# Kernel tuning notes

Measured on AMD Instinct MI355X. Metric: run time of the kernel, lower is better.

## Reference

```python
import jax, jax.numpy as jnp
import numpy as np

B, T, H, NH = 2, 2048, 1024, 16
HD = H // NH


def setup_inputs() -> dict:
    key = jax.random.key(0)
    ks = jax.random.split(key, 12)
    s = 1.0 / np.sqrt(H)
    inp = {
        "q": jax.random.normal(ks[0], (B, T, H), jnp.float32),
        "k": jax.random.normal(ks[1], (B, T, H), jnp.float32),
        "v": jax.random.normal(ks[2], (B, T, H), jnp.float32),
        "mask": jnp.tril(jnp.ones((T, T), jnp.int32))[None, None],  # causal [1,1,T,T]
        "w_q": jax.random.normal(ks[3], (H, H), jnp.float32) * s,
        "b_q": jax.random.normal(ks[4], (H,), jnp.float32) * 0.01,
        "w_k": jax.random.normal(ks[5], (H, H), jnp.float32) * s,
        "b_k": jax.random.normal(ks[6], (H,), jnp.float32) * 0.01,
        "w_v": jax.random.normal(ks[7], (H, H), jnp.float32) * s,
        "b_v": jax.random.normal(ks[8], (H,), jnp.float32) * 0.01,
        "w_o": jax.random.normal(ks[9], (H, H), jnp.float32) * s,
        "b_o": jax.random.normal(ks[10], (H,), jnp.float32) * 0.01,
    }
    return inp


def reference(q, k, v, mask, w_q, b_q, w_k, b_k, w_v, b_v, w_o, b_o):
    def split_heads(x):
        Bx, Tx, _ = x.shape
        return x.reshape(Bx, Tx, NH, HD).transpose(0, 2, 1, 3)  # [B,NH,T,HD]

    Q = split_heads(q @ w_q.T + b_q)
    K = split_heads(k @ w_k.T + b_k)
    V = split_heads(v @ w_v.T + b_v)

    scores = jnp.einsum("bhqd,bhkd->bhqk", Q, K) / np.sqrt(HD).astype(np.float32)
    scores = jnp.where(mask == 0, jnp.float32(-1e9), scores)
    weights = jax.nn.softmax(scores, axis=-1)  # dropout prob = 0.0
    out = jnp.einsum("bhqk,bhkd->bhqd", weights, V)
    out = out.transpose(0, 2, 1, 3).reshape(q.shape[0], q.shape[1], H)
    return out @ w_o.T + b_o
```

## Files before the change

### kernel.cpp

```cpp
#include <hip/hip_runtime.h>
#include <hip/hip_bf16.h>

#define Bb 2
#define Tt 2048
#define Hh 1024
#define NHh 16

typedef short bf16x8 __attribute__((ext_vector_type(8)));
typedef float f32x4 __attribute__((ext_vector_type(4)));
typedef unsigned short u16;
typedef unsigned int u32;
typedef u16 u16x4v __attribute__((ext_vector_type(4)));
typedef u32 u32x2v __attribute__((ext_vector_type(2)));

#define QK_SCALE 0.180336880f

#if __has_builtin(__builtin_amdgcn_exp2f)
__device__ __forceinline__ float exp2_fast(float x) { return __builtin_amdgcn_exp2f(x); }
#else
__device__ __forceinline__ float exp2_fast(float x) { return __expf(x * 0.69314718f); }
#endif

__device__ __forceinline__ u16 f2b(float x) {
  unsigned u = __builtin_bit_cast(unsigned, x);
  u += 0x7FFFu + ((u >> 16) & 1u);
  return (u16)(u >> 16);
}

__device__ __forceinline__ u32 cvt_pk(float lo, float hi) {
  u32 r;
  asm("v_cvt_pk_bf16_f32 %0, %1, %2" : "=v"(r) : "v"(lo), "v"(hi));
  return r;
}

__global__ __launch_bounds__(256) void cvt_all_kernel(
    const float* __restrict__ q, const float* __restrict__ k, const float* __restrict__ v,
    const float* __restrict__ wq, const float* __restrict__ wk,
    const float* __restrict__ wv, const float* __restrict__ wo,
    u16* __restrict__ qb, u16* __restrict__ kb, u16* __restrict__ vb,
    u16* __restrict__ wqb, u16* __restrict__ wkb, u16* __restrict__ wvb,
    u16* __restrict__ wob, int n4_in, int n4_w) {
  const int which = blockIdx.y;
  const float* src;
  u16* dst;
  int n4;
  float sc = 1.0f;
  switch (which) {
    case 0: src = q;  dst = qb;  n4 = n4_in; break;
    case 1: src = k;  dst = kb;  n4 = n4_in; break;
    case 2: src = v;  dst = vb;  n4 = n4_in; break;
    case 3: src = wq; dst = wqb; n4 = n4_w; sc = QK_SCALE; break;
    case 4: src = wk; dst = wkb; n4 = n4_w; break;
    case 5: src = wv; dst = wvb; n4 = n4_w; break;
    default: src = wo; dst = wob; n4 = n4_w; break;
  }
  int i = blockIdx.x * blockDim.x + threadIdx.x;
  int stride = gridDim.x * blockDim.x;
  for (; i < n4; i += stride) {
    float4 vv = ((const float4*)src)[i];
    u16x4v o;
    o.x = f2b(vv.x * sc); o.y = f2b(vv.y * sc); o.z = f2b(vv.z * sc); o.w = f2b(vv.w * sc);
    ((u16x4v*)dst)[i] = o;
  }
}

template<int NF, int MODE>
__device__ __forceinline__ void gemm_body(const u16* __restrict__ A,
                                          const u16* __restrict__ W,
                                          const float* __restrict__ bias, float bscale,
                                          void* __restrict__ Cout,
                                          u16* lA, u16* lB, int mt, int nt) {
  const int tid = threadIdx.x;
  const int lane = tid & 63;
  const int wid = tid >> 6;
  const int wr = wid >> 1, wc = wid & 1;
  const int g = lane >> 4, fr = lane & 15;
  constexpr int NT = NF * 32;

  f32x4 acc[4][NF];
#pragma unroll
  for (int m = 0; m < 4; ++m)
#pragma unroll
    for (int n = 0; n < NF; ++n) acc[m][n] = (f32x4){0.f, 0.f, 0.f, 0.f};

  const int srow = tid >> 3;
  const int scol = (tid & 7) * 8;

  bf16x8 ra[4], rb[NF];
#pragma unroll
  for (int ps = 0; ps < 4; ++ps)
    ra[ps] = *(const bf16x8*)(A + (size_t)(mt * 128 + ps * 32 + srow) * Hh + scol);
#pragma unroll
  for (int ps = 0; ps < NF; ++ps)
    rb[ps] = *(const bf16x8*)(W + (size_t)(nt * NT + ps * 32 + srow) * Hh + scol);
#pragma unroll
  for (int ps = 0; ps < 4; ++ps) {
    int r = ps * 32 + srow;
    *(bf16x8*)((char*)lA + r * 128 + ((scol * 2) ^ ((r & 7) << 4))) = ra[ps];
  }
#pragma unroll
  for (int ps = 0; ps < NF; ++ps) {
    int r = ps * 32 + srow;
    *(bf16x8*)((char*)lB + r * 128 + ((scol * 2) ^ ((r & 7) << 4))) = rb[ps];
  }
  __syncthreads();

  for (int kt = 0; kt < Hh; kt += 64) {
    if (kt + 64 < Hh) {
#pragma unroll
      for (int ps = 0; ps < 4; ++ps)
        ra[ps] = *(const bf16x8*)(A + (size_t)(mt * 128 + ps * 32 + srow) * Hh + kt + 64 + scol);
#pragma unroll
      for (int ps = 0; ps < NF; ++ps)
        rb[ps] = *(const bf16x8*)(W + (size_t)(nt * NT + ps * 32 + srow) * Hh + kt + 64 + scol);
    }
    bf16x8 af[4][2], bfv[NF][2];
#pragma unroll
    for (int m = 0; m < 4; ++m)
#pragma unroll
      for (int ks = 0; ks < 2; ++ks) {
        int r = wr * 64 + m * 16 + fr;
        af[m][ks] = *(const bf16x8*)((const char*)lA + r * 128 + ((ks * 64 + g * 16) ^ ((r & 7) << 4)));
      }
#pragma unroll
    for (int n = 0; n < NF; ++n)
#pragma unroll
      for (int ks = 0; ks < 2; ++ks) {
        int r = wc * (NT / 2) + n * 16 + fr;
        bfv[n][ks] = *(const bf16x8*)((const char*)lB + r * 128 + ((ks * 64 + g * 16) ^ ((r & 7) << 4)));
      }
#pragma unroll
    for (int m = 0; m < 4; ++m)
#pragma unroll
      for (int n = 0; n < NF; ++n)
#pragma unroll
        for (int ks = 0; ks < 2; ++ks)
          acc[m][n] = __builtin_amdgcn_mfma_f32_16x16x32_bf16(af[m][ks], bfv[n][ks],
                                                              acc[m][n], 0, 0, 0);
    if (kt + 64 < Hh) {
      __syncthreads();
#pragma unroll
      for (int ps = 0; ps < 4; ++ps) {
        int r = ps * 32 + srow;
        *(bf16x8*)((char*)lA + r * 128 + ((scol * 2) ^ ((r & 7) << 4))) = ra[ps];
      }
#pragma unroll
      for (int ps = 0; ps < NF; ++ps) {
        int r = ps * 32 + srow;
        *(bf16x8*)((char*)lB + r * 128 + ((scol * 2) ^ ((r & 7) << 4))) = rb[ps];
      }
      __syncthreads();
    }
  }

#pragma unroll
  for (int n = 0; n < NF; ++n) {
    int Cc = nt * NT + wc * (NT / 2) + n * 16 + fr;
    float bv = bias[Cc] * bscale;
#pragma unroll
    for (int m = 0; m < 4; ++m) {
#pragma unroll
      for (int j = 0; j < 4; ++j) {
        int R = mt * 128 + wr * 64 + m * 16 + g * 4 + j;
        float val = acc[m][n][j] + bv;
        if constexpr (MODE == 0) {
          int bb = R >> 11, t = R & (Tt - 1);
          int h = Cc >> 6, d = Cc & 63;
          ((u16*)Cout)[(((size_t)(bb * NHh + h) * Tt + t) << 6) + d] = f2b(val);
        } else if constexpr (MODE == 2) {
          int bb = R >> 11, t = R & (Tt - 1);
          int h = Cc >> 6, d = Cc & 63;
          ((u16*)Cout)[(((size_t)(bb * NHh + h) * 64 + d) << 11) + t] = f2b(val);
        } else {
          ((float*)Cout)[(size_t)R * Hh + Cc] = val;
        }
      }
    }
  }
}

__global__ __launch_bounds__(256, 4) void proj_qkv_kernel(
    const u16* __restrict__ qb, const u16* __restrict__ kb, const u16* __restrict__ vb,
    const u16* __restrict__ wqb, const u16* __restrict__ wkb, const u16* __restrict__ wvb,
    const float* __restrict__ biq, const float* __restrict__ bik, const float* __restrict__ biv,
    u16* __restrict__ Qp, u16* __restrict__ Kp, u16* __restrict__ Vt) {
  __shared__ u16 lA[128 * 64];
  __shared__ u16 lB[64 * 64];
  const int id = blockIdx.x;
  const int j = id >> 3;
  const int slot = (id & 7) + 8 * (j >> 4);
  const int nt = j & 15;
  const int z = slot >> 5, mt = slot & 31;
  if (z == 0)      gemm_body<2, 0>(qb, wqb, biq, QK_SCALE, Qp, lA, lB, mt, nt);
  else if (z == 1) gemm_body<2, 0>(kb, wkb, bik, 1.0f, Kp, lA, lB, mt, nt);
  else             gemm_body<2, 2>(vb, wvb, biv, 1.0f, Vt, lA, lB, mt, nt);
}

__global__ __launch_bounds__(256, 2) void gemm_out_kernel(
    const u16* __restrict__ A, const u16* __restrict__ W,
    const float* __restrict__ bias, float* __restrict__ Cout) {
  __shared__ u16 lA[128 * 64];
  __shared__ u16 lB[64 * 64];
  const int id = blockIdx.x;
  const int j = id >> 3;
  const int mt = (id & 7) + 8 * (j >> 4);
  const int nt = j & 15;
  gemm_body<2, 1>(A, W, bias, 1.0f, Cout, lA, lB, mt, nt);
}

__global__ __launch_bounds__(256, 6) void attn_kernel(const u16* __restrict__ Qp,
                                                      const u16* __restrict__ Kp,
                                                      const u16* __restrict__ Vt,
                                                      u16* __restrict__ AO) {
  __shared__ u16 lK[64 * 64];
  __shared__ u16 lV[64 * 64];
  __shared__ u16 lP[64 * 64];
  const int tid = threadIdx.x;
  const int lane = tid & 63;
  const int w = tid >> 6;
  const int g = lane >> 4, fr = lane & 15;
  const int L = blockIdx.x;
  const int i = L & 255, k4 = L >> 8;
  const int bh = i & 31, s8 = i >> 5;
  const int t2 = s8 * 2 + (k4 >> 1);
  const int qt = (k4 & 1) ? (31 - t2) : t2;
  const int q0 = qt * 64;

  bf16x8 qf[2];
  {
    const u16* qrow = Qp + (((size_t)bh * Tt + q0 + w * 16 + fr) << 6) + g * 8;
    qf[0] = *(const bf16x8*)(qrow);
    qf[1] = *(const bf16x8*)(qrow + 32);
  }

  const int srow = tid >> 3;
  const int scol = (tid & 7) * 8;
  const int sswz = (scol * 2) ^ ((srow & 7) << 4);

  bf16x8 rk[2], rv[2];
#pragma unroll
  for (int ps = 0; ps < 2; ++ps) {
    rk[ps] = *(const bf16x8*)(Kp + (((size_t)bh * Tt + ps * 32 + srow) << 6) + scol);
    rv[ps] = *(const bf16x8*)(Vt + (((size_t)bh * 64 + ps * 32 + srow) << 11) + scol);
  }
#pragma unroll
  for (int ps = 0; ps < 2; ++ps) {
    *(bf16x8*)((char*)lK + (ps * 32 + srow) * 128 + sswz) = rk[ps];
    *(bf16x8*)((char*)lV + (ps * 32 + srow) * 128 + sswz) = rv[ps];
  }
  __syncthreads();

  float m_r = -1e30f, l_r = 0.f;
  f32x4 acc[4];
#pragma unroll
  for (int nd = 0; nd < 4; ++nd) acc[nd] = (f32x4){0.f, 0.f, 0.f, 0.f};

  const int prow = w * 16 + fr;
  const int psw = (prow & 7) << 4;
  const int qoff = w * 16 + fr;

  for (int jt = 0; jt <= qt; ++jt) {
    if (jt < qt) {
#pragma unroll
      for (int ps = 0; ps < 2; ++ps) {
        rk[ps] = *(const bf16x8*)(Kp + (((size_t)bh * Tt + (jt + 1) * 64 + ps * 32 + srow) << 6) + scol);
        rv[ps] = *(const bf16x8*)(Vt + (((size_t)bh * 64 + ps * 32 + srow) << 11) + (jt + 1) * 64 + scol);
      }
    }
    f32x4 s[4];
    __builtin_amdgcn_s_setprio(1);
#pragma unroll
    for (int n = 0; n < 4; ++n) {
      s[n] = (f32x4){0.f, 0.f, 0.f, 0.f};
      int rbase = (n * 16 + fr) * 128;
      int rsw = (fr & 7) << 4;
#pragma unroll
      for (int ks = 0; ks < 2; ++ks) {
        bf16x8 ak = *(const bf16x8*)((const char*)lK + rbase + ((ks * 64 + g * 16) ^ rsw));
        s[n] = __builtin_amdgcn_mfma_f32_16x16x32_bf16(ak, qf[ks], s[n], 0, 0, 0);
      }
    }
    __builtin_amdgcn_s_setprio(0);

    float tm = -1e30f;
    if (jt == qt) {
#pragma unroll
      for (int n = 0; n < 4; ++n)
#pragma unroll
        for (int r = 0; r < 4; ++r) {
          if (n * 16 + g * 4 + r > qoff) s[n][r] = -1e30f;
          tm = fmaxf(tm, s[n][r]);
        }
    } else {
#pragma unroll
      for (int n = 0; n < 4; ++n)
#pragma unroll
        for (int r = 0; r < 4; ++r) tm = fmaxf(tm, s[n][r]);
    }
    tm = fmaxf(tm, __shfl_xor(tm, 16));
    tm = fmaxf(tm, __shfl_xor(tm, 32));
    if (!__all(tm <= m_r + 8.0f)) {
      float mn = fmaxf(m_r, tm);
      float sc = exp2_fast(m_r - mn);
      m_r = mn;
      l_r *= sc;
      float scj[4];
#pragma unroll
      for (int j = 0; j < 4; ++j) scj[j] = __shfl(sc, g * 4 + j);
#pragma unroll
      for (int nd = 0; nd < 4; ++nd)
#pragma unroll
        for (int j = 0; j < 4; ++j) acc[nd][j] *= scj[j];
    }
    float rs = 0.f;
    u32 pw[4][2];
#pragma unroll
    for (int n = 0; n < 4; ++n) {
      float p0 = exp2_fast(s[n][0] - m_r);
      float p1 = exp2_fast(s[n][1] - m_r);
      float p2 = exp2_fast(s[n][2] - m_r);
      float p3 = exp2_fast(s[n][3] - m_r);
      rs += (p0 + p1) + (p2 + p3);
      pw[n][0] = cvt_pk(p0, p1);
      pw[n][1] = cvt_pk(p2, p3);
    }
    rs += __shfl_xor(rs, 16);
    rs += __shfl_xor(rs, 32);
    l_r += rs;
    bf16x8 pa[2];
    {
      char* base = (char*)lP + prow * 128;
#pragma unroll
      for (int n = 0; n < 4; ++n)
        *(u32x2v*)(base + ((32 * n + 8 * g) ^ psw)) = (u32x2v){pw[n][0], pw[n][1]};
#pragma unroll
      for (int ks = 0; ks < 2; ++ks)
        pa[ks] = *(const bf16x8*)(base + ((ks * 64 + g * 16) ^ psw));
    }
    __builtin_amdgcn_s_setprio(1);
#pragma unroll
    for (int nd = 0; nd < 4; ++nd) {
      int rbase = (nd * 16 + fr) * 128;
      int rsw = (fr & 7) << 4;
#pragma unroll
      for (int ks = 0; ks < 2; ++ks) {
        bf16x8 bv = *(const bf16x8*)((const char*)lV + rbase + ((ks * 64 + g * 16) ^ rsw));
        acc[nd] = __builtin_amdgcn_mfma_f32_16x16x32_bf16(pa[ks], bv, acc[nd], 0, 0, 0);
      }
    }
    __builtin_amdgcn_s_setprio(0);
    if (jt < qt) {
      __syncthreads();
#pragma unroll
      for (int ps = 0; ps < 2; ++ps) {
        *(bf16x8*)((char*)lK + (ps * 32 + srow) * 128 + sswz) = rk[ps];
        *(bf16x8*)((char*)lV + (ps * 32 + srow) * 128 + sswz) = rv[ps];
      }
      __syncthreads();
    }
  }

  const int b = bh >> 4, hh = bh & 15;
  float lj[4];
#pragma unroll
  for (int j = 0; j < 4; ++j) lj[j] = __shfl(l_r, g * 4 + j);
#pragma unroll
  for (int j = 0; j < 4; ++j) {
    float inv = 1.0f / lj[j];
    int qq = q0 + w * 16 + g * 4 + j;
    size_t base = (((size_t)b * Tt + qq) << 10) + hh * 64;
#pragma unroll
    for (int nd = 0; nd < 4; ++nd)
      AO[base + nd * 16 + fr] = f2b(acc[nd][j] * inv);
  }
}

extern "C" void kernel_launch(void* const* d_in, const int* in_sizes, int n_in,
                              void* d_out, int out_size, void* d_ws, size_t ws_size,
                              hipStream_t stream) {
  const float* q   = (const float*)d_in[0];
  const float* k   = (const float*)d_in[1];
  const float* v   = (const float*)d_in[2];
  const float* wq  = (const float*)d_in[4];
  const float* bq  = (const float*)d_in[5];
  const float* wk  = (const float*)d_in[6];
  const float* bk  = (const float*)d_in[7];
  const float* wv  = (const float*)d_in[8];
  const float* bv  = (const float*)d_in[9];
  const float* wo  = (const float*)d_in[10];
  const float* bo  = (const float*)d_in[11];

  char* ws = (char*)d_ws;
  const size_t SZB = (size_t)Bb * Tt * Hh * 2;
  const size_t WB  = (size_t)Hh * Hh * 2;
  u16* qb  = (u16*)(ws);
  u16* kb  = (u16*)(ws + SZB);
  u16* vb  = (u16*)(ws + 2 * SZB);
  u16* wqb = (u16*)(ws + 3 * SZB);
  u16* wkb = (u16*)(ws + 3 * SZB + WB);
  u16* wvb = (u16*)(ws + 3 * SZB + 2 * WB);
  u16* wob = (u16*)(ws + 3 * SZB + 3 * WB);
  u16* Qp  = (u16*)(ws + 3 * SZB + 4 * WB);
  u16* Kp  = (u16*)(ws + 4 * SZB + 4 * WB);
  u16* Vt  = (u16*)(ws + 5 * SZB + 4 * WB);
  u16* AO  = qb;

  const int N4_IN = (Bb * Tt * Hh) / 4;
  const int N4_W  = (Hh * Hh) / 4;
  cvt_all_kernel<<<dim3(512, 7), 256, 0, stream>>>(
      q, k, v, wq, wk, wv, wo, qb, kb, vb, wqb, wkb, wvb, wob, N4_IN, N4_W);

  proj_qkv_kernel<<<dim3(1536), 256, 0, stream>>>(
      qb, kb, vb, wqb, wkb, wvb, bq, bk, bv, Qp, Kp, Vt);

  attn_kernel<<<dim3(1024), 256, 0, stream>>>(Qp, Kp, Vt, AO);

  gemm_out_kernel<<<dim3(512), 256, 0, stream>>>(
      AO, wob, bo, (float*)d_out);
}
```

Measured before the change: 126.3 us.

## Split long causal query tiles across KV chunks with merge, double-buffer K/V LDS

Query tiles 16-31 of causal attention are split into two KV ranges (0-15 and 16-qt), giving 1536 blocks in place of 1024 with more even per-block work. Split blocks write unnormalized bf16 partial outputs plus running max/sum, and a new merge kernel combines them into AO. K/V shared memory is double-buffered, which removes one __syncthreads per iteration. The cost is an extra launch, extra global traffic for the partials, an added bf16 rounding of partial outputs, and larger LDS use with launch bounds lowered from 6 to 4 blocks.

```diff
diff --git a/kernel.cpp b/kernel.cpp
--- a/kernel.cpp
+++ b/kernel.cpp
@@ -25,6 +25,9 @@
   unsigned u = __builtin_bit_cast(unsigned, x);
   u += 0x7FFFu + ((u >> 16) & 1u);
   return (u16)(u >> 16);
+}
+__device__ __forceinline__ float b2f(u16 x) {
+  return __builtin_bit_cast(float, (u32)x << 16);
 }
 
 __device__ __forceinline__ u32 cvt_pk(float lo, float hi) {
@@ -208,22 +211,34 @@
   gemm_body<2, 1>(A, W, bias, 1.0f, Cout, lA, lB, mt, nt);
 }
 
-__global__ __launch_bounds__(256, 6) void attn_kernel(const u16* __restrict__ Qp,
+__global__ __launch_bounds__(256, 4) void attn_kernel(const u16* __restrict__ Qp,
                                                       const u16* __restrict__ Kp,
                                                       const u16* __restrict__ Vt,
-                                                      u16* __restrict__ AO) {
-  __shared__ u16 lK[64 * 64];
-  __shared__ u16 lV[64 * 64];
+                                                      u16* __restrict__ AO,
+                                                      u16* __restrict__ Obuf,
+                                                      float2* __restrict__ MLbuf) {
+  __shared__ u16 lK[2][64 * 64];
+  __shared__ u16 lV[2][64 * 64];
   __shared__ u16 lP[64 * 64];
   const int tid = threadIdx.x;
   const int lane = tid & 63;
   const int w = tid >> 6;
   const int g = lane >> 4, fr = lane & 15;
-  const int L = blockIdx.x;
-  const int i = L & 255, k4 = L >> 8;
-  const int bh = i & 31, s8 = i >> 5;
-  const int t2 = s8 * 2 + (k4 >> 1);
-  const int qt = (k4 & 1) ? (31 - t2) : t2;
+
+  const int id = blockIdx.x;
+  int bh, qt, kv0, kv1, chunk = 0;
+  bool split;
+  if (id < 512) {
+    bh = id & 31; qt = 16 + (id >> 5);
+    kv0 = 0; kv1 = 15; split = true;
+  } else {
+    int r = id - 512;
+    int d = 16 - (r >> 6);
+    int p = r & 63;
+    bh = p & 31;
+    if (p < 32) { qt = d - 1;  kv0 = 0;  kv1 = qt; split = false; }
+    else        { qt = 15 + d; kv0 = 16; kv1 = qt; split = true; chunk = 1; }
+  }
   const int q0 = qt * 64;
 
   bf16x8 qf[2];
@@ -240,13 +255,13 @@
   bf16x8 rk[2], rv[2];
 #pragma unroll
   for (int ps = 0; ps < 2; ++ps) {
-    rk[ps] = *(const bf16x8*)(Kp + (((size_t)bh * Tt + ps * 32 + srow) << 6) + scol);
-    rv[ps] = *(const bf16x8*)(Vt + (((size_t)bh * 64 + ps * 32 + srow) << 11) + scol);
+    rk[ps] = *(const bf16x8*)(Kp + (((size_t)bh * Tt + kv0 * 64 + ps * 32 + srow) << 6) + scol);
+    rv[ps] = *(const bf16x8*)(Vt + (((size_t)bh * 64 + ps * 32 + srow) << 11) + kv0 * 64 + scol);
   }
 #pragma unroll
   for (int ps = 0; ps < 2; ++ps) {
-    *(bf16x8*)((char*)lK + (ps * 32 + srow) * 128 + sswz) = rk[ps];
-    *(bf16x8*)((char*)lV + (ps * 32 + srow) * 128 + sswz) = rv[ps];
+    *(bf16x8*)((char*)lK[0] + (ps * 32 + srow) * 128 + sswz) = rk[ps];
+    *(bf16x8*)((char*)lV[0] + (ps * 32 + srow) * 128 + sswz) = rv[ps];
   }
   __syncthreads();
 
@@ -259,8 +274,10 @@
   const int psw = (prow & 7) << 4;
   const int qoff = w * 16 + fr;
 
-  for (int jt = 0; jt <= qt; ++jt) {
-    if (jt < qt) {
+  for (int jt = kv0; jt <= kv1; ++jt) {
+    const char* bK = (const char*)lK[jt & 1];
+    const char* bV = (const char*)lV[jt & 1];
+    if (jt < kv1) {
 #pragma unroll
       for (int ps = 0; ps < 2; ++ps) {
         rk[ps] = *(const bf16x8*)(Kp + (((size_t)bh * Tt + (jt + 1) * 64 + ps * 32 + srow) << 6) + scol);
@@ -276,7 +293,7 @@
       int rsw = (fr & 7) << 4;
 #pragma unroll
       for (int ks = 0; ks < 2; ++ks) {
-        bf16x8 ak = *(const bf16x8*)((const char*)lK + rbase + ((ks * 64 + g * 16) ^ rsw));
+        bf16x8 ak = *(const bf16x8*)(bK + rbase + ((ks * 64 + g * 16) ^ rsw));
         s[n] = __builtin_amdgcn_mfma_f32_16x16x32_bf16(ak, qf[ks], s[n], 0, 0, 0);
       }
     }
@@ -344,34 +361,78 @@
       int rsw = (fr & 7) << 4;
 #pragma unroll
       for (int ks = 0; ks < 2; ++ks) {
-        bf16x8 bv = *(const bf16x8*)((const char*)lV + rbase + ((ks * 64 + g * 16) ^ rsw));
+        bf16x8 bv = *(const bf16x8*)(bV + rbase + ((ks * 64 + g * 16) ^ rsw));
         acc[nd] = __builtin_amdgcn_mfma_f32_16x16x32_bf16(pa[ks], bv, acc[nd], 0, 0, 0);
       }
     }
     __builtin_amdgcn_s_setprio(0);
-    if (jt < qt) {
+    if (jt < kv1) {
+#pragma unroll
+      for (int ps = 0; ps < 2; ++ps) {
+        *(bf16x8*)((char*)lK[(jt + 1) & 1] + (ps * 32 + srow) * 128 + sswz) = rk[ps];
+        *(bf16x8*)((char*)lV[(jt + 1) & 1] + (ps * 32 + srow) * 128 + sswz) = rv[ps];
+      }
       __syncthreads();
-#pragma unroll
-      for (int ps = 0; ps < 2; ++ps) {
-        *(bf16x8*)((char*)lK + (ps * 32 + srow) * 128 + sswz) = rk[ps];
-        *(bf16x8*)((char*)lV + (ps * 32 + srow) * 128 + sswz) = rv[ps];
-      }
-      __syncthreads();
-    }
-  }
-
+    }
+  }
+
+  if (!split) {
+    const int b = bh >> 4, hh = bh & 15;
+    float lj[4];
+#pragma unroll
+    for (int j = 0; j < 4; ++j) lj[j] = __shfl(l_r, g * 4 + j);
+#pragma unroll
+    for (int j = 0; j < 4; ++j) {
+      float inv = 1.0f / lj[j];
+      int qq = q0 + w * 16 + g * 4 + j;
+      size_t base = (((size_t)b * Tt + qq) << 10) + hh * 64;
+#pragma unroll
+      for (int nd = 0; nd < 4; ++nd)
+        AO[base + nd * 16 + fr] = f2b(acc[nd][j] * inv);
+    }
+  } else {
+    const int pidx = ((bh * 16 + (qt - 16)) << 1) + chunk;
+    if (g == 0) MLbuf[pidx * 64 + w * 16 + fr] = make_float2(m_r, l_r);
+    u16* ob = Obuf + (size_t)pidx * 4096;
+#pragma unroll
+    for (int j = 0; j < 4; ++j) {
+      int row = w * 16 + g * 4 + j;
+#pragma unroll
+      for (int nd = 0; nd < 4; ++nd)
+        ob[row * 64 + nd * 16 + fr] = f2b(acc[nd][j]);
+    }
+  }
+}
+
+__global__ __launch_bounds__(256) void merge_kernel(const u16* __restrict__ Obuf,
+                                                    const float2* __restrict__ MLbuf,
+                                                    u16* __restrict__ AO) {
+  const int row_id = blockIdx.x * 256 + threadIdx.x;
+  const int bh = row_id >> 10;
+  const int qs = (row_id >> 6) & 15;
+  const int row = row_id & 63;
+  const int tile = bh * 16 + qs;
+  float2 ml0 = MLbuf[(tile * 2 + 0) * 64 + row];
+  float2 ml1 = MLbuf[(tile * 2 + 1) * 64 + row];
+  float M = fmaxf(ml0.x, ml1.x);
+  float w0 = exp2_fast(ml0.x - M);
+  float w1 = exp2_fast(ml1.x - M);
+  float inv = 1.0f / (w0 * ml0.y + w1 * ml1.y);
+  const u16* o0 = Obuf + (size_t)(tile * 2 + 0) * 4096 + row * 64;
+  const u16* o1 = Obuf + (size_t)(tile * 2 + 1) * 4096 + row * 64;
+  const int qt = 16 + qs;
+  const int qq = qt * 64 + row;
   const int b = bh >> 4, hh = bh & 15;
-  float lj[4];
-#pragma unroll
-  for (int j = 0; j < 4; ++j) lj[j] = __shfl(l_r, g * 4 + j);
-#pragma unroll
-  for (int j = 0; j < 4; ++j) {
-    float inv = 1.0f / lj[j];
-    int qq = q0 + w * 16 + g * 4 + j;
-    size_t base = (((size_t)b * Tt + qq) << 10) + hh * 64;
-#pragma unroll
-    for (int nd = 0; nd < 4; ++nd)
-      AO[base + nd * 16 + fr] = f2b(acc[nd][j] * inv);
+  u16* dst = AO + (((size_t)b * Tt + qq) << 10) + hh * 64;
+#pragma unroll
+  for (int c = 0; c < 8; ++c) {
+    bf16x8 v0 = *(const bf16x8*)(o0 + c * 8);
+    bf16x8 v1 = *(const bf16x8*)(o1 + c * 8);
+    bf16x8 o;
+#pragma unroll
+    for (int e = 0; e < 8; ++e)
+      o[e] = (short)f2b((w0 * b2f((u16)v0[e]) + w1 * b2f((u16)v1[e])) * inv);
+    *(bf16x8*)(dst + c * 8) = o;
   }
 }
 
@@ -404,6 +465,8 @@
   u16* Kp  = (u16*)(ws + 4 * SZB + 4 * WB);
   u16* Vt  = (u16*)(ws + 5 * SZB + 4 * WB);
   u16* AO  = qb;
+  u16* Obuf = kb;
+  float2* MLbuf = (float2*)vb;
 
   const int N4_IN = (Bb * Tt * Hh) / 4;
   const int N4_W  = (Hh * Hh) / 4;
@@ -413,7 +476,9 @@
   proj_qkv_kernel<<<dim3(1536), 256, 0, stream>>>(
       qb, kb, vb, wqb, wkb, wvb, bq, bk, bv, Qp, Kp, Vt);
 
-  attn_kernel<<<dim3(1024), 256, 0, stream>>>(Qp, Kp, Vt, AO);
+  attn_kernel<<<dim3(1536), 256, 0, stream>>>(Qp, Kp, Vt, AO, Obuf, MLbuf);
+
+  merge_kernel<<<dim3(128), 256, 0, stream>>>(Obuf, MLbuf, AO);
 
   gemm_out_kernel<<<dim3(512), 256, 0, stream>>>(
       AO, wob, bo, (float*)d_out);
```

New measurement: 113.7 us. 10.0% less time.
